# Performance work log

Measured on AMD Instinct MI355X. Metric: run time of the kernel, lower is better.

The kernel has to match this reference:

```python
import jax, jax.numpy as jnp
import numpy as np

NEG_INF = -9e15  # matches -9000000000000000.0 in torch code
ALPHA = 0.2      # LeakyReLU negative slope


def setup_inputs() -> dict:
    key = jax.random.key(0)
    k1, k2, k3, k4 = jax.random.split(key, 4)
    B, N, Fin, Fout = 8, 2048, 256, 256
    h = jax.random.normal(k1, (B, N, Fin), dtype=jnp.float32)
    adj = jax.random.randint(k2, (B, N, N), 0, 2, dtype=jnp.int32)
    W = jax.random.normal(k3, (Fin, Fout), dtype=jnp.float32) * 0.05
    a = jax.random.normal(k4, (2 * Fout, 1), dtype=jnp.float32) * 0.05
    return {"h": h, "adj": adj, "W": W, "a": a}


def reference(h, adj, W, a):
    # h: [B,N,Fin], adj: [B,N,N], W: [Fin,Fout], a: [2*Fout,1]
    Fout = W.shape[1]
    Wh = jnp.matmul(h, W)                       # [B,N,Fout]
    # Decompose concat-based additive score: e_ij = LReLU(a1.Wh_i + a2.Wh_j)
    a1 = a[:Fout, 0]                            # source-node part
    a2 = a[Fout:, 0]                            # target-node part
    s1 = jnp.einsum('bnf,f->bn', Wh, a1)        # [B,N]
    s2 = jnp.einsum('bnf,f->bn', Wh, a2)        # [B,N]
    e = jax.nn.leaky_relu(s1[:, :, None] + s2[:, None, :], negative_slope=ALPHA)  # [B,N,N]
    attn = jnp.where(adj > 0, e, NEG_INF)
    attn = jax.nn.softmax(attn, axis=2)          # masked softmax over neighbors
    # dropout omitted (deterministic eval-mode reference)
    h_prime = jnp.matmul(attn, Wh)               # [B,N,Fout]
    return h_prime
```

## Files before the change

### kernel.cpp

```cpp
#include <hip/hip_runtime.h>
#include <cstdint>

#define ALPHA 0.2f

constexpr int NB = 8;
constexpr int NN = 2048;
constexpr int NF = 256;

typedef __attribute__((ext_vector_type(8))) short bf16x8;
typedef __attribute__((ext_vector_type(4))) float f32x4;

__device__ __forceinline__ float bf2f(unsigned short u) {
    union { unsigned int i; float f; } v;
    v.i = ((unsigned int)u) << 16;
    return v.f;
}
__device__ __forceinline__ unsigned short f2bf(float f) {
    union { float f; unsigned int i; } v;
    v.f = f;
    v.i += 0x7fffu + ((v.i >> 16) & 1);
    return (unsigned short)(v.i >> 16);
}
__device__ __forceinline__ unsigned int pk2bf(float lo, float hi) {
    union { float f; unsigned int u; } a, b;
    a.f = lo; b.f = hi;
    return __builtin_amdgcn_perm(b.u + 0x8000u, a.u + 0x8000u, 0x07060302u);
}

__global__ __launch_bounds__(256) void k_wt(const float* __restrict__ W,
                                            unsigned short* __restrict__ WT,
                                            float* __restrict__ s1,
                                            float* __restrict__ s2) {
    const int t = threadIdx.x;
    const int gid = blockIdx.x * 256 + t;
    s1[gid] = 0.f;
    s2[gid] = 0.f;
    const int k = blockIdx.x * 4 + (t >> 6);
    const int f0 = (t & 63) * 4;
    const float4 w = *(const float4*)&W[k * NF + f0];
    WT[(f0 + 0) * NF + k] = f2bf(w.x);
    WT[(f0 + 1) * NF + k] = f2bf(w.y);
    WT[(f0 + 2) * NF + k] = f2bf(w.z);
    WT[(f0 + 3) * NF + k] = f2bf(w.w);
}

__global__ __launch_bounds__(256, 4) void k_wh(const float* __restrict__ h,
                                               const unsigned short* __restrict__ WT,
                                               const float* __restrict__ a,
                                               unsigned short* __restrict__ WhT,
                                               float* __restrict__ s1,
                                               float* __restrict__ s2) {
    __shared__ __align__(16) unsigned short As[64][72];
    __shared__ __align__(16) unsigned short Bs[64][72];
    const int tid = threadIdx.x;
    const int lane = tid & 63;
    const int l16 = lane & 15;
    const int quad = lane >> 4;
    const int wave = tid >> 6;

    const int p = blockIdx.x;
    const int xcd = p & 7;
    const int q = p >> 3;
    const int rowTile = xcd + (q >> 2) * 8;
    const int row0 = rowTile * 64;
    const int col0 = (q & 3) * 64;

    const int bb = row0 >> 11;
    const int n0 = row0 & (NN - 1);
    const int mb = (wave & 1) * 32;
    const int nb = (wave >> 1) * 32;

    f32x4 acc[2][2];
#pragma unroll
    for (int mf = 0; mf < 2; ++mf)
#pragma unroll
        for (int nf = 0; nf < 2; ++nf) acc[mf][nf] = (f32x4){0.f, 0.f, 0.f, 0.f};

    const int r0 = tid >> 4;
    const int k4 = (tid & 15) * 4;
    const int f0w = tid >> 3;
    const int k8 = (tid & 7) * 8;

    const float* hP = &h[(size_t)(row0 + r0) * NF + k4];
    const unsigned short* wP = &WT[(size_t)(col0 + f0w) * NF + k8];

    float4 h0, h1, h2, h3;
    uint4 wv0, wv1;

#define LOADW(K0)                                                      \
    do {                                                               \
        h0 = *(const float4*)&hP[(size_t)(0 * 16) * NF + (K0)];        \
        h1 = *(const float4*)&hP[(size_t)(1 * 16) * NF + (K0)];        \
        h2 = *(const float4*)&hP[(size_t)(2 * 16) * NF + (K0)];        \
        h3 = *(const float4*)&hP[(size_t)(3 * 16) * NF + (K0)];        \
        wv0 = *(const uint4*)&wP[(K0)];                                \
        wv1 = *(const uint4*)&wP[(size_t)32 * NF + (K0)];              \
    } while (0)

    LOADW(0);

    for (int k0 = 0; k0 < NF; k0 += 64) {
        ushort4 o;
        o.x = f2bf(h0.x); o.y = f2bf(h0.y); o.z = f2bf(h0.z); o.w = f2bf(h0.w);
        *(ushort4*)&As[r0 + 0][k4] = o;
        o.x = f2bf(h1.x); o.y = f2bf(h1.y); o.z = f2bf(h1.z); o.w = f2bf(h1.w);
        *(ushort4*)&As[r0 + 16][k4] = o;
        o.x = f2bf(h2.x); o.y = f2bf(h2.y); o.z = f2bf(h2.z); o.w = f2bf(h2.w);
        *(ushort4*)&As[r0 + 32][k4] = o;
        o.x = f2bf(h3.x); o.y = f2bf(h3.y); o.z = f2bf(h3.z); o.w = f2bf(h3.w);
        *(ushort4*)&As[r0 + 48][k4] = o;
        *(uint4*)&Bs[f0w][k8] = wv0;
        *(uint4*)&Bs[f0w + 32][k8] = wv1;
        __syncthreads();
        if (k0 + 64 < NF) LOADW(k0 + 64);
#pragma unroll
        for (int ks = 0; ks < 64; ks += 32) {
            bf16x8 av[2], bv[2];
#pragma unroll
            for (int mf = 0; mf < 2; ++mf)
                av[mf] = *(const bf16x8*)&As[mb + mf * 16 + l16][ks + quad * 8];
#pragma unroll
            for (int nf = 0; nf < 2; ++nf)
                bv[nf] = *(const bf16x8*)&Bs[nb + nf * 16 + l16][ks + quad * 8];
#pragma unroll
            for (int mf = 0; mf < 2; ++mf)
#pragma unroll
                for (int nf = 0; nf < 2; ++nf)
                    acc[mf][nf] = __builtin_amdgcn_mfma_f32_16x16x32_bf16(
                        av[mf], bv[nf], acc[mf][nf], 0, 0, 0);
        }
        __syncthreads();
    }
#undef LOADW

#pragma unroll
    for (int mf = 0; mf < 2; ++mf) {
#pragma unroll
        for (int nf = 0; nf < 2; ++nf) {
            const size_t f = col0 + nb + nf * 16 + l16;
            const int nr = n0 + mb + mf * 16 + quad * 4;
            ushort4 o;
            o.x = f2bf(acc[mf][nf][0]);
            o.y = f2bf(acc[mf][nf][1]);
            o.z = f2bf(acc[mf][nf][2]);
            o.w = f2bf(acc[mf][nf][3]);
            *(ushort4*)&WhT[((size_t)bb * NF + f) * NN + nr] = o;
        }
    }

    float a1v[2], a2v[2];
#pragma unroll
    for (int nf = 0; nf < 2; ++nf) {
        const int f = col0 + nb + nf * 16 + l16;
        a1v[nf] = a[f];
        a2v[nf] = a[NF + f];
    }
#pragma unroll
    for (int mf = 0; mf < 2; ++mf) {
#pragma unroll
        for (int r = 0; r < 4; ++r) {
            float p1 = acc[mf][0][r] * a1v[0] + acc[mf][1][r] * a1v[1];
            float p2 = acc[mf][0][r] * a2v[0] + acc[mf][1][r] * a2v[1];
            p1 += __shfl_xor(p1, 1); p2 += __shfl_xor(p2, 1);
            p1 += __shfl_xor(p1, 2); p2 += __shfl_xor(p2, 2);
            p1 += __shfl_xor(p1, 4); p2 += __shfl_xor(p2, 4);
            p1 += __shfl_xor(p1, 8); p2 += __shfl_xor(p2, 8);
            if (l16 == 0) {
                const int n = n0 + mb + mf * 16 + quad * 4 + r;
                atomicAdd(&s1[bb * NN + n], p1);
                atomicAdd(&s2[bb * NN + n], p2);
            }
        }
    }
}

__global__ __launch_bounds__(256, 3) void k_attn(const unsigned short* __restrict__ WhT,
                                                 const int* __restrict__ adj,
                                                 const float* __restrict__ s1g,
                                                 const float* __restrict__ s2g,
                                                 float* __restrict__ out) {
    __shared__ __align__(16) unsigned short WhsT[256][72];
    __shared__ __align__(16) unsigned short Pb[32][72];
    __shared__ float l_s[32];

    const int tid = threadIdx.x;
    const int lane = tid & 63;
    const int l16 = lane & 15;
    const int quad = lane >> 4;
    const int wave = tid >> 6;
    const int bb = blockIdx.x & 7;
    const int i0 = (blockIdx.x >> 3) * 32;

    f32x4 acc[2][4];
#pragma unroll
    for (int m = 0; m < 2; ++m)
#pragma unroll
        for (int nf = 0; nf < 4; ++nf) acc[m][nf] = (f32x4){0.f, 0.f, 0.f, 0.f};

    const size_t whtBase = (size_t)bb * NF * NN;
    const size_t adjBase = (size_t)bb * NN * NN;
    const float* s2b = s2g + bb * NN;

    const int whF = tid >> 3;
    const int whK = (tid & 7) * 8;
    const int pIr = tid >> 4;
    const int pKq = (tid & 15) * 4;

    const unsigned short* whP = &WhT[whtBase + (size_t)whF * NN + whK];
    const int* adjP0 = &adj[adjBase + (size_t)(i0 + pIr) * NN + pKq];
    const int* adjP1 = adjP0 + 16 * NN;
    const float* s2P = &s2b[pKq];

    const float s1v0 = s1g[bb * NN + i0 + pIr];
    const float s1v1 = s1g[bb * NN + i0 + pIr + 16];
    float lsum0 = 0.f, lsum1 = 0.f;

    uint4 w0, w1, w2, w3, w4, w5, w6, w7;
    int4 am0, am1;
    float4 sv0;

#define LOAD_TILE(J0)                                                         \
    do {                                                                      \
        const int j0_ = (J0);                                                 \
        w0 = *(const uint4*)&whP[(size_t)(0 * 32) * NN + j0_];                \
        w1 = *(const uint4*)&whP[(size_t)(1 * 32) * NN + j0_];                \
        w2 = *(const uint4*)&whP[(size_t)(2 * 32) * NN + j0_];                \
        w3 = *(const uint4*)&whP[(size_t)(3 * 32) * NN + j0_];                \
        w4 = *(const uint4*)&whP[(size_t)(4 * 32) * NN + j0_];                \
        w5 = *(const uint4*)&whP[(size_t)(5 * 32) * NN + j0_];                \
        w6 = *(const uint4*)&whP[(size_t)(6 * 32) * NN + j0_];                \
        w7 = *(const uint4*)&whP[(size_t)(7 * 32) * NN + j0_];                \
        am0 = *(const int4*)&adjP0[j0_];                                      \
        am1 = *(const int4*)&adjP1[j0_];                                      \
        sv0 = *(const float4*)&s2P[j0_];                                      \
    } while (0)

    LOAD_TILE(0);

    for (int t = 0; t < NN / 64; ++t) {
        *(uint4*)&WhsT[whF + 0 * 32][whK] = w0;
        *(uint4*)&WhsT[whF + 1 * 32][whK] = w1;
        *(uint4*)&WhsT[whF + 2 * 32][whK] = w2;
        *(uint4*)&WhsT[whF + 3 * 32][whK] = w3;
        *(uint4*)&WhsT[whF + 4 * 32][whK] = w4;
        *(uint4*)&WhsT[whF + 5 * 32][whK] = w5;
        *(uint4*)&WhsT[whF + 6 * 32][whK] = w6;
        *(uint4*)&WhsT[whF + 7 * 32][whK] = w7;
        {
            float x0 = s1v0 + sv0.x, x1 = s1v0 + sv0.y;
            float x2 = s1v0 + sv0.z, x3 = s1v0 + sv0.w;
            x0 = fmaxf(x0, ALPHA * x0);
            x1 = fmaxf(x1, ALPHA * x1);
            x2 = fmaxf(x2, ALPHA * x2);
            x3 = fmaxf(x3, ALPHA * x3);
            const float p0 = am0.x > 0 ? __expf(x0) : 0.f;
            const float p1 = am0.y > 0 ? __expf(x1) : 0.f;
            const float p2 = am0.z > 0 ? __expf(x2) : 0.f;
            const float p3 = am0.w > 0 ? __expf(x3) : 0.f;
            uint2 pk;
            pk.x = pk2bf(p0, p1);
            pk.y = pk2bf(p2, p3);
            *(uint2*)&Pb[pIr][pKq] = pk;
            lsum0 += (p0 + p1) + (p2 + p3);
        }
        {
            float x0 = s1v1 + sv0.x, x1 = s1v1 + sv0.y;
            float x2 = s1v1 + sv0.z, x3 = s1v1 + sv0.w;
            x0 = fmaxf(x0, ALPHA * x0);
            x1 = fmaxf(x1, ALPHA * x1);
            x2 = fmaxf(x2, ALPHA * x2);
            x3 = fmaxf(x3, ALPHA * x3);
            const float p0 = am1.x > 0 ? __expf(x0) : 0.f;
            const float p1 = am1.y > 0 ? __expf(x1) : 0.f;
            const float p2 = am1.z > 0 ? __expf(x2) : 0.f;
            const float p3 = am1.w > 0 ? __expf(x3) : 0.f;
            uint2 pk;
            pk.x = pk2bf(p0, p1);
            pk.y = pk2bf(p2, p3);
            *(uint2*)&Pb[pIr + 16][pKq] = pk;
            lsum1 += (p0 + p1) + (p2 + p3);
        }
        __syncthreads();
        if (t + 1 < NN / 64) LOAD_TILE((t + 1) * 64);
        const int f0 = wave * 64;
#pragma unroll
        for (int k0 = 0; k0 < 64; k0 += 32) {
            bf16x8 af[2];
#pragma unroll
            for (int m = 0; m < 2; ++m)
                af[m] = *(const bf16x8*)&Pb[m * 16 + l16][k0 + quad * 8];
#pragma unroll
            for (int nf = 0; nf < 4; ++nf) {
                const bf16x8 bfr =
                    *(const bf16x8*)&WhsT[f0 + nf * 16 + l16][k0 + quad * 8];
#pragma unroll
                for (int m = 0; m < 2; ++m)
                    acc[m][nf] = __builtin_amdgcn_mfma_f32_16x16x32_bf16(
                        af[m], bfr, acc[m][nf], 0, 0, 0);
            }
        }
        __syncthreads();
    }
#undef LOAD_TILE

    lsum0 += __shfl_xor(lsum0, 1);
    lsum0 += __shfl_xor(lsum0, 2);
    lsum0 += __shfl_xor(lsum0, 4);
    lsum0 += __shfl_xor(lsum0, 8);
    lsum1 += __shfl_xor(lsum1, 1);
    lsum1 += __shfl_xor(lsum1, 2);
    lsum1 += __shfl_xor(lsum1, 4);
    lsum1 += __shfl_xor(lsum1, 8);
    if ((tid & 15) == 0) {
        l_s[pIr] = 1.0f / lsum0;
        l_s[pIr + 16] = 1.0f / lsum1;
    }
    __syncthreads();

    const int f0 = wave * 64;
#pragma unroll
    for (int m = 0; m < 2; ++m) {
#pragma unroll
        for (int r = 0; r < 4; ++r) {
            const int row = m * 16 + quad * 4 + r;
            const float inv = l_s[row];
#pragma unroll
            for (int nf = 0; nf < 4; ++nf) {
                out[((size_t)bb * NN + i0 + row) * NF + f0 + nf * 16 + l16] =
                    acc[m][nf][r] * inv;
            }
        }
    }
}

extern "C" void kernel_launch(void* const* d_in, const int* in_sizes, int n_in,
                              void* d_out, int out_size, void* d_ws, size_t ws_size,
                              hipStream_t stream) {
    const float* h = (const float*)d_in[0];
    const int* adj = (const int*)d_in[1];
    const float* W = (const float*)d_in[2];
    const float* a = (const float*)d_in[3];
    float* out = (float*)d_out;

    unsigned short* WhT = (unsigned short*)d_ws;
    float* s1 = (float*)((char*)d_ws + (size_t)NB * NN * NF * sizeof(unsigned short));
    float* s2 = s1 + (size_t)NB * NN;
    unsigned short* WT = (unsigned short*)(s2 + (size_t)NB * NN);

    k_wt<<<dim3(64), dim3(256), 0, stream>>>(W, WT, s1, s2);
    k_wh<<<dim3((NB * NN / 64) * (NF / 64)), dim3(256), 0, stream>>>(h, WT, a, WhT, s1, s2);
    k_attn<<<dim3(NB * (NN / 32)), dim3(256), 0, stream>>>(WhT, adj, s1, s2, out);
}
```

Measured before the change: 237.2 us.

## Load Wh MFMA B-fragments directly from global, double-buffer P tile

Drops the shared-memory staging of the transposed Wh tile. Each wave now loads its MFMA B operands straight from global memory into registers, in the fragment layout. The P tile becomes double-buffered in LDS with two register sets for loads, so each iteration needs one barrier instead of two and the LDS write/read traffic for Wh is gone. The cost is that each block loads Wh without sharing it across waves, which is more redundant global/L2 traffic, and register pressure rises enough that occupancy is lowered to 2 blocks per SM.

```diff
diff --git a/kernel.cpp b/kernel.cpp
--- a/kernel.cpp
+++ b/kernel.cpp
@@ -174,13 +174,12 @@
     }
 }
 
-__global__ __launch_bounds__(256, 3) void k_attn(const unsigned short* __restrict__ WhT,
+__global__ __launch_bounds__(256, 2) void k_attn(const unsigned short* __restrict__ WhT,
                                                  const int* __restrict__ adj,
                                                  const float* __restrict__ s1g,
                                                  const float* __restrict__ s2g,
                                                  float* __restrict__ out) {
-    __shared__ __align__(16) unsigned short WhsT[256][72];
-    __shared__ __align__(16) unsigned short Pb[32][72];
+    __shared__ __align__(16) unsigned short Pb[2][32][72];
     __shared__ float l_s[32];
 
     const int tid = threadIdx.x;
@@ -199,109 +198,136 @@
 
     const size_t whtBase = (size_t)bb * NF * NN;
     const size_t adjBase = (size_t)bb * NN * NN;
-    const float* s2b = s2g + bb * NN;
-
-    const int whF = tid >> 3;
-    const int whK = (tid & 7) * 8;
+
     const int pIr = tid >> 4;
     const int pKq = (tid & 15) * 4;
-
-    const unsigned short* whP = &WhT[whtBase + (size_t)whF * NN + whK];
     const int* adjP0 = &adj[adjBase + (size_t)(i0 + pIr) * NN + pKq];
     const int* adjP1 = adjP0 + 16 * NN;
-    const float* s2P = &s2b[pKq];
+    const float* s2P = &s2g[bb * NN + pKq];
 
     const float s1v0 = s1g[bb * NN + i0 + pIr];
     const float s1v1 = s1g[bb * NN + i0 + pIr + 16];
     float lsum0 = 0.f, lsum1 = 0.f;
 
-    uint4 w0, w1, w2, w3, w4, w5, w6, w7;
-    int4 am0, am1;
-    float4 sv0;
-
-#define LOAD_TILE(J0)                                                         \
+    const int f0 = wave * 64;
+    const unsigned short* whB0 = &WhT[whtBase + (size_t)(f0 + 0 * 16 + l16) * NN + quad * 8];
+    const unsigned short* whB1 = whB0 + (size_t)16 * NN;
+    const unsigned short* whB2 = whB0 + (size_t)32 * NN;
+    const unsigned short* whB3 = whB0 + (size_t)48 * NN;
+
+    uint4 bA0, bA1, bA2, bA3, bA4, bA5, bA6, bA7;
+    uint4 bB0, bB1, bB2, bB3, bB4, bB5, bB6, bB7;
+    int4 amA0, amA1, amB0, amB1;
+    float4 svA, svB;
+
+#define LOADSET(P0, P1, P2, P3, P4, P5, P6, P7, AM0, AM1, SV, J0)             \
     do {                                                                      \
-        const int j0_ = (J0);                                                 \
-        w0 = *(const uint4*)&whP[(size_t)(0 * 32) * NN + j0_];                \
-        w1 = *(const uint4*)&whP[(size_t)(1 * 32) * NN + j0_];                \
-        w2 = *(const uint4*)&whP[(size_t)(2 * 32) * NN + j0_];                \
-        w3 = *(const uint4*)&whP[(size_t)(3 * 32) * NN + j0_];                \
-        w4 = *(const uint4*)&whP[(size_t)(4 * 32) * NN + j0_];                \
-        w5 = *(const uint4*)&whP[(size_t)(5 * 32) * NN + j0_];                \
-        w6 = *(const uint4*)&whP[(size_t)(6 * 32) * NN + j0_];                \
-        w7 = *(const uint4*)&whP[(size_t)(7 * 32) * NN + j0_];                \
-        am0 = *(const int4*)&adjP0[j0_];                                      \
-        am1 = *(const int4*)&adjP1[j0_];                                      \
-        sv0 = *(const float4*)&s2P[j0_];                                      \
+        const int j_ = (J0);                                                  \
+        P0 = *(const uint4*)&whB0[j_];                                        \
+        P1 = *(const uint4*)&whB1[j_];                                        \
+        P2 = *(const uint4*)&whB2[j_];                                        \
+        P3 = *(const uint4*)&whB3[j_];                                        \
+        P4 = *(const uint4*)&whB0[j_ + 32];                                   \
+        P5 = *(const uint4*)&whB1[j_ + 32];                                   \
+        P6 = *(const uint4*)&whB2[j_ + 32];                                   \
+        P7 = *(const uint4*)&whB3[j_ + 32];                                   \
+        AM0 = *(const int4*)&adjP0[j_];                                       \
+        AM1 = *(const int4*)&adjP1[j_];                                       \
+        SV = *(const float4*)&s2P[j_];                                        \
     } while (0)
 
-    LOAD_TILE(0);
-
-    for (int t = 0; t < NN / 64; ++t) {
-        *(uint4*)&WhsT[whF + 0 * 32][whK] = w0;
-        *(uint4*)&WhsT[whF + 1 * 32][whK] = w1;
-        *(uint4*)&WhsT[whF + 2 * 32][whK] = w2;
-        *(uint4*)&WhsT[whF + 3 * 32][whK] = w3;
-        *(uint4*)&WhsT[whF + 4 * 32][whK] = w4;
-        *(uint4*)&WhsT[whF + 5 * 32][whK] = w5;
-        *(uint4*)&WhsT[whF + 6 * 32][whK] = w6;
-        *(uint4*)&WhsT[whF + 7 * 32][whK] = w7;
-        {
-            float x0 = s1v0 + sv0.x, x1 = s1v0 + sv0.y;
-            float x2 = s1v0 + sv0.z, x3 = s1v0 + sv0.w;
-            x0 = fmaxf(x0, ALPHA * x0);
-            x1 = fmaxf(x1, ALPHA * x1);
-            x2 = fmaxf(x2, ALPHA * x2);
-            x3 = fmaxf(x3, ALPHA * x3);
-            const float p0 = am0.x > 0 ? __expf(x0) : 0.f;
-            const float p1 = am0.y > 0 ? __expf(x1) : 0.f;
-            const float p2 = am0.z > 0 ? __expf(x2) : 0.f;
-            const float p3 = am0.w > 0 ? __expf(x3) : 0.f;
-            uint2 pk;
-            pk.x = pk2bf(p0, p1);
-            pk.y = pk2bf(p2, p3);
-            *(uint2*)&Pb[pIr][pKq] = pk;
-            lsum0 += (p0 + p1) + (p2 + p3);
-        }
-        {
-            float x0 = s1v1 + sv0.x, x1 = s1v1 + sv0.y;
-            float x2 = s1v1 + sv0.z, x3 = s1v1 + sv0.w;
-            x0 = fmaxf(x0, ALPHA * x0);
-            x1 = fmaxf(x1, ALPHA * x1);
-            x2 = fmaxf(x2, ALPHA * x2);
-            x3 = fmaxf(x3, ALPHA * x3);
-            const float p0 = am1.x > 0 ? __expf(x0) : 0.f;
-            const float p1 = am1.y > 0 ? __expf(x1) : 0.f;
-            const float p2 = am1.z > 0 ? __expf(x2) : 0.f;
-            const float p3 = am1.w > 0 ? __expf(x3) : 0.f;
-            uint2 pk;
-            pk.x = pk2bf(p0, p1);
-            pk.y = pk2bf(p2, p3);
-            *(uint2*)&Pb[pIr + 16][pKq] = pk;
-            lsum1 += (p0 + p1) + (p2 + p3);
-        }
+#define PCOMP(AM0, AM1, SV, BUF)                                              \
+    do {                                                                      \
+        float x0 = s1v0 + SV.x, x1 = s1v0 + SV.y;                             \
+        float x2 = s1v0 + SV.z, x3 = s1v0 + SV.w;                             \
+        x0 = fmaxf(x0, ALPHA * x0);                                           \
+        x1 = fmaxf(x1, ALPHA * x1);                                           \
+        x2 = fmaxf(x2, ALPHA * x2);                                           \
+        x3 = fmaxf(x3, ALPHA * x3);                                           \
+        const float p0 = AM0.x > 0 ? __expf(x0) : 0.f;                        \
+        const float p1 = AM0.y > 0 ? __expf(x1) : 0.f;                        \
+        const float p2 = AM0.z > 0 ? __expf(x2) : 0.f;                        \
+        const float p3 = AM0.w > 0 ? __expf(x3) : 0.f;                        \
+        uint2 pk;                                                             \
+        pk.x = pk2bf(p0, p1);                                                 \
+        pk.y = pk2bf(p2, p3);                                                 \
+        *(uint2*)&Pb[BUF][pIr][pKq] = pk;                                     \
+        lsum0 += (p0 + p1) + (p2 + p3);                                       \
+        float y0 = s1v1 + SV.x, y1 = s1v1 + SV.y;                             \
+        float y2 = s1v1 + SV.z, y3 = s1v1 + SV.w;                             \
+        y0 = fmaxf(y0, ALPHA * y0);                                           \
+        y1 = fmaxf(y1, ALPHA * y1);                                           \
+        y2 = fmaxf(y2, ALPHA * y2);                                           \
+        y3 = fmaxf(y3, ALPHA * y3);                                           \
+        const float q0 = AM1.x > 0 ? __expf(y0) : 0.f;                        \
+        const float q1 = AM1.y > 0 ? __expf(y1) : 0.f;                        \
+        const float q2 = AM1.z > 0 ? __expf(y2) : 0.f;                        \
+        const float q3 = AM1.w > 0 ? __expf(y3) : 0.f;                        \
+        pk.x = pk2bf(q0, q1);                                                 \
+        pk.y = pk2bf(q2, q3);                                                 \
+        *(uint2*)&Pb[BUF][pIr + 16][pKq] = pk;                                \
+        lsum1 += (q0 + q1) + (q2 + q3);                                       \
+    } while (0)
+
+#define MFMA_PH(P0, P1, P2, P3, P4, P5, P6, P7, BUF)                          \
+    do {                                                                      \
+        bf16x8 af0 = *(const bf16x8*)&Pb[BUF][l16][quad * 8];                 \
+        bf16x8 af1 = *(const bf16x8*)&Pb[BUF][16 + l16][quad * 8];            \
+        acc[0][0] = __builtin_amdgcn_mfma_f32_16x16x32_bf16(                  \
+            af0, *(const bf16x8*)&P0, acc[0][0], 0, 0, 0);                    \
+        acc[1][0] = __builtin_amdgcn_mfma_f32_16x16x32_bf16(                  \
+            af1, *(const bf16x8*)&P0, acc[1][0], 0, 0, 0);                    \
+        acc[0][1] = __builtin_amdgcn_mfma_f32_16x16x32_bf16(                  \
+            af0, *(const bf16x8*)&P1, acc[0][1], 0, 0, 0);                    \
+        acc[1][1] = __builtin_amdgcn_mfma_f32_16x16x32_bf16(                  \
+            af1, *(const bf16x8*)&P1, acc[1][1], 0, 0, 0);                    \
+        acc[0][2] = __builtin_amdgcn_mfma_f32_16x16x32_bf16(                  \
+            af0, *(const bf16x8*)&P2, acc[0][2], 0, 0, 0);                    \
+        acc[1][2] = __builtin_amdgcn_mfma_f32_16x16x32_bf16(                  \
+            af1, *(const bf16x8*)&P2, acc[1][2], 0, 0, 0);                    \
+        acc[0][3] = __builtin_amdgcn_mfma_f32_16x16x32_bf16(                  \
+            af0, *(const bf16x8*)&P3, acc[0][3], 0, 0, 0);                    \
+        acc[1][3] = __builtin_amdgcn_mfma_f32_16x16x32_bf16(                  \
+            af1, *(const bf16x8*)&P3, acc[1][3], 0, 0, 0);                    \
+        af0 = *(const bf16x8*)&Pb[BUF][l16][32 + quad * 8];                   \
+        af1 = *(const bf16x8*)&Pb[BUF][16 + l16][32 + quad * 8];              \
+        acc[0][0] = __builtin_amdgcn_mfma_f32_16x16x32_bf16(                  \
+            af0, *(const bf16x8*)&P4, acc[0][0], 0, 0, 0);                    \
+        acc[1][0] = __builtin_amdgcn_mfma_f32_16x16x32_bf16(                  \
+            af1, *(const bf16x8*)&P4, acc[1][0], 0, 0, 0);                    \
+        acc[0][1] = __builtin_amdgcn_mfma_f32_16x16x32_bf16(                  \
+            af0, *(const bf16x8*)&P5, acc[0][1], 0, 0, 0);                    \
+        acc[1][1] = __builtin_amdgcn_mfma_f32_16x16x32_bf16(                  \
+            af1, *(const bf16x8*)&P5, acc[1][1], 0, 0, 0);                    \
+        acc[0][2] = __builtin_amdgcn_mfma_f32_16x16x32_bf16(                  \
+            af0, *(const bf16x8*)&P6, acc[0][2], 0, 0, 0);                    \
+        acc[1][2] = __builtin_amdgcn_mfma_f32_16x16x32_bf16(                  \
+            af1, *(const bf16x8*)&P6, acc[1][2], 0, 0, 0);                    \
+        acc[0][3] = __builtin_amdgcn_mfma_f32_16x16x32_bf16(                  \
+            af0, *(const bf16x8*)&P7, acc[0][3], 0, 0, 0);                    \
+        acc[1][3] = __builtin_amdgcn_mfma_f32_16x16x32_bf16(                  \
+            af1, *(const bf16x8*)&P7, acc[1][3], 0, 0, 0);                    \
+    } while (0)
+
+    LOADSET(bA0, bA1, bA2, bA3, bA4, bA5, bA6, bA7, amA0, amA1, svA, 0);
+
+    for (int tt = 0; tt < NN / 128; ++tt) {
+        const int t0 = 2 * tt;
+        PCOMP(amA0, amA1, svA, 0);
         __syncthreads();
-        if (t + 1 < NN / 64) LOAD_TILE((t + 1) * 64);
-        const int f0 = wave * 64;
-#pragma unroll
-        for (int k0 = 0; k0 < 64; k0 += 32) {
-            bf16x8 af[2];
-#pragma unroll
-            for (int m = 0; m < 2; ++m)
-                af[m] = *(const bf16x8*)&Pb[m * 16 + l16][k0 + quad * 8];
-#pragma unroll
-            for (int nf = 0; nf < 4; ++nf) {
-                const bf16x8 bfr =
-                    *(const bf16x8*)&WhsT[f0 + nf * 16 + l16][k0 + quad * 8];
-#pragma unroll
-                for (int m = 0; m < 2; ++m)
-                    acc[m][nf] = __builtin_amdgcn_mfma_f32_16x16x32_bf16(
-                        af[m], bfr, acc[m][nf], 0, 0, 0);
-            }
-        }
+        LOADSET(bB0, bB1, bB2, bB3, bB4, bB5, bB6, bB7, amB0, amB1, svB,
+                (t0 + 1) * 64);
+        MFMA_PH(bA0, bA1, bA2, bA3, bA4, bA5, bA6, bA7, 0);
+        PCOMP(amB0, amB1, svB, 1);
         __syncthreads();
-    }
-#undef LOAD_TILE
+        if (tt < NN / 128 - 1)
+            LOADSET(bA0, bA1, bA2, bA3, bA4, bA5, bA6, bA7, amA0, amA1, svA,
+                    (t0 + 2) * 64);
+        MFMA_PH(bB0, bB1, bB2, bB3, bB4, bB5, bB6, bB7, 1);
+    }
+#undef LOADSET
+#undef PCOMP
+#undef MFMA_PH
 
     lsum0 += __shfl_xor(lsum0, 1);
     lsum0 += __shfl_xor(lsum0, 2);
@@ -317,7 +343,6 @@
     }
     __syncthreads();
 
-    const int f0 = wave * 64;
 #pragma unroll
     for (int m = 0; m < 2; ++m) {
 #pragma unroll
```

Result: slower. 262.5 us (+10.7%).

## Prefetch adjacency rows into shared-memory bitmask before attention loop

Applied to the files above, without the earlier changes.

Each block now streams its 32 adjacency rows up front with wide coalesced loads and packs them into a 32x64-word bitmask in shared memory. The main loop reads mask bits from LDS instead of issuing per-tile int4 global loads of adj. This front-loads the dominant HBM read and shrinks the per-iteration register and load pressure. In exchange, the adjacency read no longer overlaps with the MMA loop, and the kernel uses 8 KB more shared memory, which may affect occupancy.

```diff
diff --git a/kernel.cpp b/kernel.cpp
--- a/kernel.cpp
+++ b/kernel.cpp
@@ -181,6 +181,7 @@
                                                  float* __restrict__ out) {
     __shared__ __align__(16) unsigned short WhsT[256][72];
     __shared__ __align__(16) unsigned short Pb[32][72];
+    __shared__ unsigned int adjbits[32][64];
     __shared__ float l_s[32];
 
     const int tid = threadIdx.x;
@@ -191,32 +192,51 @@
     const int bb = blockIdx.x & 7;
     const int i0 = (blockIdx.x >> 3) * 32;
 
-    f32x4 acc[2][4];
-#pragma unroll
-    for (int m = 0; m < 2; ++m)
-#pragma unroll
-        for (int nf = 0; nf < 4; ++nf) acc[m][nf] = (f32x4){0.f, 0.f, 0.f, 0.f};
-
     const size_t whtBase = (size_t)bb * NF * NN;
     const size_t adjBase = (size_t)bb * NN * NN;
-    const float* s2b = s2g + bb * NN;
+
+#pragma unroll 2
+    for (int r8 = 0; r8 < 8; ++r8) {
+        const int row = wave * 8 + r8;
+        const int* ap = &adj[adjBase + (size_t)(i0 + row) * NN];
+#pragma unroll
+        for (int c = 0; c < 4; ++c) {
+            const int col = c * 512 + lane * 8;
+            const int4 v0 = *(const int4*)&ap[col];
+            const int4 v1 = *(const int4*)&ap[col + 4];
+            unsigned int b = (v0.x > 0 ? 1u : 0u) | (v0.y > 0 ? 2u : 0u) |
+                             (v0.z > 0 ? 4u : 0u) | (v0.w > 0 ? 8u : 0u) |
+                             (v1.x > 0 ? 16u : 0u) | (v1.y > 0 ? 32u : 0u) |
+                             (v1.z > 0 ? 64u : 0u) | (v1.w > 0 ? 128u : 0u);
+            const unsigned int u = b | (__shfl_down(b, 1) << 8) |
+                                   (__shfl_down(b, 2) << 16) |
+                                   (__shfl_down(b, 3) << 24);
+            if ((lane & 3) == 0) adjbits[row][c * 16 + (lane >> 2)] = u;
+        }
+    }
+    __syncthreads();
+
+    f32x4 acc[2][4];
+#pragma unroll
+    for (int m = 0; m < 2; ++m)
+#pragma unroll
+        for (int nf = 0; nf < 4; ++nf) acc[m][nf] = (f32x4){0.f, 0.f, 0.f, 0.f};
 
     const int whF = tid >> 3;
     const int whK = (tid & 7) * 8;
     const int pIr = tid >> 4;
     const int pKq = (tid & 15) * 4;
+    const int wOff = pKq >> 5;
+    const int bitsh = pKq & 31;
 
     const unsigned short* whP = &WhT[whtBase + (size_t)whF * NN + whK];
-    const int* adjP0 = &adj[adjBase + (size_t)(i0 + pIr) * NN + pKq];
-    const int* adjP1 = adjP0 + 16 * NN;
-    const float* s2P = &s2b[pKq];
+    const float* s2P = &s2g[bb * NN + pKq];
 
     const float s1v0 = s1g[bb * NN + i0 + pIr];
     const float s1v1 = s1g[bb * NN + i0 + pIr + 16];
     float lsum0 = 0.f, lsum1 = 0.f;
 
     uint4 w0, w1, w2, w3, w4, w5, w6, w7;
-    int4 am0, am1;
     float4 sv0;
 
 #define LOAD_TILE(J0)                                                         \
@@ -230,8 +250,6 @@
         w5 = *(const uint4*)&whP[(size_t)(5 * 32) * NN + j0_];                \
         w6 = *(const uint4*)&whP[(size_t)(6 * 32) * NN + j0_];                \
         w7 = *(const uint4*)&whP[(size_t)(7 * 32) * NN + j0_];                \
-        am0 = *(const int4*)&adjP0[j0_];                                      \
-        am1 = *(const int4*)&adjP1[j0_];                                      \
         sv0 = *(const float4*)&s2P[j0_];                                      \
     } while (0)
 
@@ -246,6 +264,8 @@
         *(uint4*)&WhsT[whF + 5 * 32][whK] = w5;
         *(uint4*)&WhsT[whF + 6 * 32][whK] = w6;
         *(uint4*)&WhsT[whF + 7 * 32][whK] = w7;
+        const unsigned int m0 = adjbits[pIr][2 * t + wOff] >> bitsh;
+        const unsigned int m1 = adjbits[pIr + 16][2 * t + wOff] >> bitsh;
         {
             float x0 = s1v0 + sv0.x, x1 = s1v0 + sv0.y;
             float x2 = s1v0 + sv0.z, x3 = s1v0 + sv0.w;
@@ -253,10 +273,10 @@
             x1 = fmaxf(x1, ALPHA * x1);
             x2 = fmaxf(x2, ALPHA * x2);
             x3 = fmaxf(x3, ALPHA * x3);
-            const float p0 = am0.x > 0 ? __expf(x0) : 0.f;
-            const float p1 = am0.y > 0 ? __expf(x1) : 0.f;
-            const float p2 = am0.z > 0 ? __expf(x2) : 0.f;
-            const float p3 = am0.w > 0 ? __expf(x3) : 0.f;
+            const float p0 = (m0 & 1u) ? __expf(x0) : 0.f;
+            const float p1 = (m0 & 2u) ? __expf(x1) : 0.f;
+            const float p2 = (m0 & 4u) ? __expf(x2) : 0.f;
+            const float p3 = (m0 & 8u) ? __expf(x3) : 0.f;
             uint2 pk;
             pk.x = pk2bf(p0, p1);
             pk.y = pk2bf(p2, p3);
@@ -270,10 +290,10 @@
             x1 = fmaxf(x1, ALPHA * x1);
             x2 = fmaxf(x2, ALPHA * x2);
             x3 = fmaxf(x3, ALPHA * x3);
-            const float p0 = am1.x > 0 ? __expf(x0) : 0.f;
-            const float p1 = am1.y > 0 ? __expf(x1) : 0.f;
-            const float p2 = am1.z > 0 ? __expf(x2) : 0.f;
-            const float p3 = am1.w > 0 ? __expf(x3) : 0.f;
+            const float p0 = (m1 & 1u) ? __expf(x0) : 0.f;
+            const float p1 = (m1 & 2u) ? __expf(x1) : 0.f;
+            const float p2 = (m1 & 4u) ? __expf(x2) : 0.f;
+            const float p3 = (m1 & 8u) ? __expf(x3) : 0.f;
             uint2 pk;
             pk.x = pk2bf(p0, p1);
             pk.y = pk2bf(p2, p3);
```

New measurement: 258.8 us. +9.1%, slower.
